# Optimization experiments

Measured on AMD Instinct MI355X. Metric: run time of the kernel, lower is better.

Reference implementation:

```python
import jax, jax.numpy as jnp
import numpy as np
from jax import lax

# ---- model dims ----
NTOKEN = 60697
D_MODEL = 512
NLAYERS = 4
D_STATE = 16
D_CONV = 4
EXPAND = 2
D_INNER = EXPAND * D_MODEL      # 1024
DT_RANK = (D_MODEL + 15) // 16  # 32 (ceil(d_model/16), mamba default)
B_SZ = 4
SEQ = 2048
EPS = 1e-5


def setup_inputs() -> dict:
    key = jax.random.key(0)
    ks = jax.random.split(key, 16)
    s = 0.02
    src = jax.random.randint(ks[0], (B_SZ, SEQ), 0, NTOKEN)
    src_key_padding_mask = jnp.ones((B_SZ, SEQ), dtype=bool)
    emb_w = jax.random.normal(ks[1], (NTOKEN, D_MODEL), jnp.float32) * s
    enc_ln_w = jnp.ones((D_MODEL,), jnp.float32)
    enc_ln_b = jnp.zeros((D_MODEL,), jnp.float32)
    ln_w = jnp.ones((NLAYERS, D_MODEL), jnp.float32)
    ln_b = jnp.zeros((NLAYERS, D_MODEL), jnp.float32)
    in_proj_w = jax.random.normal(ks[2], (NLAYERS, 2 * D_INNER, D_MODEL), jnp.float32) * s
    conv_w = jax.random.normal(ks[3], (NLAYERS, D_INNER, D_CONV), jnp.float32) * 0.1
    conv_b = jnp.zeros((NLAYERS, D_INNER), jnp.float32)
    x_proj_w = jax.random.normal(ks[4], (NLAYERS, DT_RANK + 2 * D_STATE, D_INNER), jnp.float32) * s
    dt_proj_w = jax.random.normal(ks[5], (NLAYERS, D_INNER, DT_RANK), jnp.float32) * (DT_RANK ** -0.5)
    dt_proj_b = jax.random.uniform(ks[6], (NLAYERS, D_INNER), jnp.float32, -4.0, -2.0)
    # S4D real init: A = -[1..d_state], stored as log
    A_log = jnp.log(jnp.broadcast_to(jnp.arange(1, D_STATE + 1, dtype=jnp.float32),
                                     (NLAYERS, D_INNER, D_STATE)))
    D_skip = jnp.ones((NLAYERS, D_INNER), jnp.float32)
    out_proj_w = jax.random.normal(ks[7], (NLAYERS, D_MODEL, D_INNER), jnp.float32) * s / np.sqrt(NLAYERS)
    normf_w = jnp.ones((D_MODEL,), jnp.float32)
    normf_b = jnp.zeros((D_MODEL,), jnp.float32)
    return {
        'src': src, 'src_key_padding_mask': src_key_padding_mask,
        'emb_w': emb_w, 'enc_ln_w': enc_ln_w, 'enc_ln_b': enc_ln_b,
        'ln_w': ln_w, 'ln_b': ln_b, 'in_proj_w': in_proj_w,
        'conv_w': conv_w, 'conv_b': conv_b, 'x_proj_w': x_proj_w,
        'dt_proj_w': dt_proj_w, 'dt_proj_b': dt_proj_b,
        'A_log': A_log, 'D_skip': D_skip, 'out_proj_w': out_proj_w,
        'normf_w': normf_w, 'normf_b': normf_b,
    }


def _layer_norm(x, w, b, eps=EPS):
    mu = jnp.mean(x, axis=-1, keepdims=True)
    var = jnp.mean(jnp.square(x - mu), axis=-1, keepdims=True)
    return (x - mu) * lax.rsqrt(var + eps) * w + b


def _mamba_mixer(h, in_w, cw, cb, xw, dtw, dtb, A_log, D_skip, ow):
    B, L, _ = h.shape
    xz = h @ in_w.T                                   # [B,L,2*d_inner]
    x, z = jnp.split(xz, 2, axis=-1)
    # causal depthwise conv1d, kernel D_CONV
    xt = x.swapaxes(1, 2)                             # [B,d_inner,L]
    xp = jnp.pad(xt, ((0, 0), (0, 0), (D_CONV - 1, 0)))
    conv = cb[None, :, None]
    for k in range(D_CONV):
        conv = conv + cw[:, k][None, :, None] * xp[:, :, k:k + L]
    x = jax.nn.silu(conv).swapaxes(1, 2)              # [B,L,d_inner]
    xdbl = x @ xw.T                                   # [B,L,dt_rank+2*d_state]
    dt = jax.nn.softplus(xdbl[..., :DT_RANK] @ dtw.T + dtb)      # [B,L,d_inner]
    Bm = xdbl[..., DT_RANK:DT_RANK + D_STATE]                    # [B,L,d_state]
    Cm = xdbl[..., DT_RANK + D_STATE:]                           # [B,L,d_state]
    A = -jnp.exp(A_log)                               # [d_inner,d_state]

    def step(hst, inp):
        dt_t, b_t, c_t, x_t = inp                     # [B,d_inner],[B,d_state],[B,d_state],[B,d_inner]
        dA = jnp.exp(dt_t[..., None] * A)             # [B,d_inner,d_state]
        hst = dA * hst + (dt_t * x_t)[..., None] * b_t[:, None, :]
        y_t = jnp.einsum('bds,bs->bd', hst, c_t)
        return hst, y_t

    xs = (dt.swapaxes(0, 1), Bm.swapaxes(0, 1), Cm.swapaxes(0, 1), x.swapaxes(0, 1))
    h0 = jnp.zeros((B, D_INNER, D_STATE), dtype=h.dtype)
    _, ys = lax.scan(step, h0, xs)                    # ys: [L,B,d_inner]
    y = ys.swapaxes(0, 1) + x * D_skip
    y = y * jax.nn.silu(z)
    return y @ ow.T


def reference(src, src_key_padding_mask, emb_w, enc_ln_w, enc_ln_b, ln_w, ln_b,
              in_proj_w, conv_w, conv_b, x_proj_w, dt_proj_w, dt_proj_b,
              A_log, D_skip, out_proj_w, normf_w, normf_b):
    # GeneEncoder: embedding -> LayerNorm (dropout = identity in eval)
    hidden = _layer_norm(emb_w[src], enc_ln_w, enc_ln_b)
    residual = None
    for i in range(NLAYERS):  # prenorm Mamba Blocks
        residual = hidden if residual is None else hidden + residual
        hidden = _mamba_mixer(_layer_norm(residual, ln_w[i], ln_b[i]),
                              in_proj_w[i], conv_w[i], conv_b[i], x_proj_w[i],
                              dt_proj_w[i], dt_proj_b[i], A_log[i], D_skip[i],
                              out_proj_w[i])
    residual = hidden + residual
    return _layer_norm(residual, normf_w, normf_b)
```

## Files before the change

### kernel.cpp

```cpp
#include <hip/hip_runtime.h>
#include <hip/hip_bf16.h>
#include <math.h>

#define NTOKEN 60697
#define D_MODEL 512
#define NLAYERS 4
#define D_STATE 16
#define D_CONV 4
#define D_INNER 1024
#define DT_RANK 32
#define B_SZ 4
#define SEQ 2048
#define EPS 1e-5f
#define NROWS (B_SZ * SEQ)
#define CHUNK 128
#define NCHUNK (SEQ / CHUNK)
#define LOG2E 1.44269504f

typedef __bf16 bf16_t;
typedef __attribute__((ext_vector_type(8))) __bf16 bfx8;
typedef __attribute__((ext_vector_type(4))) __bf16 bfx4;
typedef __attribute__((ext_vector_type(4))) float f32x4;


__device__ __forceinline__ float fast_sigmoid(float x) {
    return 1.0f / (1.0f + __expf(-x));
}
__device__ __forceinline__ float silu(float x) {
    return x * fast_sigmoid(x);
}
__device__ __forceinline__ float softplus_f(float x) {
    return (x > 20.0f) ? x : log1pf(__expf(x));
}
__device__ __forceinline__ float exp2_fast(float x) {
    float r;
    asm("v_exp_f32 %0, %1" : "=v"(r) : "v"(x));
    return r;
}
__device__ __forceinline__ unsigned int bf16bits(float v) {
    return (unsigned int)__builtin_bit_cast(unsigned short, (bf16_t)v);
}
__device__ __forceinline__ float lo16f(unsigned int u) {
    return __builtin_bit_cast(float, u << 16);
}
__device__ __forceinline__ float hi16f(unsigned int u) {
    return __builtin_bit_cast(float, u & 0xFFFF0000u);
}

__device__ __forceinline__ void gload_lds16(const void* g, void* l) {
    __builtin_amdgcn_global_load_lds(
        (const __attribute__((address_space(1))) unsigned int*)g,
        (__attribute__((address_space(3))) unsigned int*)l, 16, 0, 0);
}

template <int CTRL>
__device__ __forceinline__ float dpp_fetch(float x) {
    int xi = __builtin_bit_cast(int, x);
    int yi = __builtin_amdgcn_update_dpp(0, xi, CTRL, 0xF, 0xF, true);
    return __builtin_bit_cast(float, yi);
}
__device__ __forceinline__ float dpp_sum16(float p) {
    p += dpp_fetch<0xB1>(p);
    p += dpp_fetch<0x4E>(p);
    p += dpp_fetch<0x141>(p);
    p += dpp_fetch<0x140>(p);
    return p;
}

__device__ __forceinline__ float blk_reduce_sum(float x, float* sbuf) {
#pragma unroll
    for (int m = 32; m >= 1; m >>= 1) x += __shfl_xor(x, m);
    int wid = threadIdx.x >> 6;
    if ((threadIdx.x & 63) == 0) sbuf[wid] = x;
    __syncthreads();
    float t = sbuf[0] + sbuf[1] + sbuf[2] + sbuf[3];
    __syncthreads();
    return t;
}

__global__ __launch_bounds__(256) void cast_bf16_kernel(
    const float* __restrict__ in, bf16_t* __restrict__ out, size_t n)
{
    size_t stride = (size_t)gridDim.x * 256 * 4;
    for (size_t i = ((size_t)blockIdx.x * 256 + threadIdx.x) * 4; i < n; i += stride) {
        float4 v = *reinterpret_cast<const float4*>(in + i);
        bfx4 o;
        o[0] = (bf16_t)v.x; o[1] = (bf16_t)v.y;
        o[2] = (bf16_t)v.z; o[3] = (bf16_t)v.w;
        *reinterpret_cast<bfx4*>(out + i) = o;
    }
}


__global__ __launch_bounds__(256) void embed_ln_kernel(
    const int* __restrict__ src, const float* __restrict__ emb,
    const float* __restrict__ w, const float* __restrict__ b,
    float* __restrict__ R)
{
    __shared__ float sbuf[4];
    int row = blockIdx.x;
    int tok = src[row];
    const float* e = emb + (size_t)tok * D_MODEL;
    int c0 = threadIdx.x, c1 = threadIdx.x + 256;
    float v0 = e[c0], v1 = e[c1];
    float mu = blk_reduce_sum(v0 + v1, sbuf) * (1.0f / D_MODEL);
    float d0 = v0 - mu, d1 = v1 - mu;
    float var = blk_reduce_sum(d0 * d0 + d1 * d1, sbuf) * (1.0f / D_MODEL);
    float rs = rsqrtf(var + EPS);
    size_t base = (size_t)row * D_MODEL;
    R[base + c0] = d0 * rs * w[c0] + b[c0];
    R[base + c1] = d1 * rs * w[c1] + b[c1];
}

__global__ __launch_bounds__(256) void add_ln_kernel(
    float* __restrict__ R, const float* __restrict__ Hadd,
    const float* __restrict__ w, const float* __restrict__ b,
    float* __restrict__ out, bf16_t* __restrict__ outb)
{
    __shared__ float sbuf[4];
    size_t base = (size_t)blockIdx.x * D_MODEL;
    int c0 = threadIdx.x, c1 = c0 + 256;
    float v0 = R[base + c0], v1 = R[base + c1];
    if (Hadd) {
        v0 += Hadd[base + c0];
        v1 += Hadd[base + c1];
        R[base + c0] = v0;
        R[base + c1] = v1;
    }
    float mu = blk_reduce_sum(v0 + v1, sbuf) * (1.0f / D_MODEL);
    float d0 = v0 - mu, d1 = v1 - mu;
    float var = blk_reduce_sum(d0 * d0 + d1 * d1, sbuf) * (1.0f / D_MODEL);
    float rs = rsqrtf(var + EPS);
    float o0 = d0 * rs * w[c0] + b[c0];
    float o1 = d1 * rs * w[c1] + b[c1];
    if (out) {
        out[base + c0] = o0;
        out[base + c1] = o1;
    }
    if (outb) {
        outb[base + c0] = (bf16_t)o0;
        outb[base + c1] = (bf16_t)o1;
    }
}

template <int EPI>
__global__ __launch_bounds__(256) void gemm_bf16_nt(
    const bf16_t* __restrict__ A, const bf16_t* __restrict__ B,
    float* __restrict__ C, int ldc, int K, const float* __restrict__ bias,
    const unsigned short* __restrict__ xcb_u16,
    unsigned int* __restrict__ dtx_u32,
    bf16_t* __restrict__ Cxb, bf16_t* __restrict__ Czb)
{
    __shared__ bf16_t As[128 * 32];
    __shared__ bf16_t Bs[128 * 32];
    int tid = threadIdx.x;
    int lane = tid & 63, wid = tid >> 6;
    int m0 = blockIdx.y * 128, n0 = blockIdx.x * 128;
    int wm = (wid >> 1) * 64, wn = (wid & 1) * 64;
    int c_lo = lane & 15;
    int khalf = lane >> 4;

    f32x4 acc[4][4];
#pragma unroll
    for (int i = 0; i < 4; i++)
#pragma unroll
        for (int j = 0; j < 4; j++)
            acc[i][j] = (f32x4){0.f, 0.f, 0.f, 0.f};

    for (int k0 = 0; k0 < K; k0 += 32) {
#pragma unroll
        for (int i = 0; i < 2; i++) {
            int c = i * 256 + tid;
            int row = c >> 2;
            int cb = (c & 3) * 16;
            int ldsoff = (i * 256 + wid * 64) * 16;
            gload_lds16((const char*)A + ((size_t)(m0 + row) * K + k0) * 2 + cb,
                        (char*)As + ldsoff);
            gload_lds16((const char*)B + ((size_t)(n0 + row) * K + k0) * 2 + cb,
                        (char*)Bs + ldsoff);
        }
        __syncthreads();

        bfx8 af[4], bfr[4];
#pragma unroll
        for (int i = 0; i < 4; i++) {
            af[i]  = *reinterpret_cast<const bfx8*>(As + (wm + i * 16 + c_lo) * 32 + khalf * 8);
            bfr[i] = *reinterpret_cast<const bfx8*>(Bs + (wn + i * 16 + c_lo) * 32 + khalf * 8);
        }
#pragma unroll
        for (int i = 0; i < 4; i++)
#pragma unroll
            for (int j = 0; j < 4; j++)
                acc[i][j] = __builtin_amdgcn_mfma_f32_16x16x32_bf16(af[i], bfr[j], acc[i][j], 0, 0, 0);
        __syncthreads();
    }

#pragma unroll
    for (int i = 0; i < 4; i++) {
#pragma unroll
        for (int j = 0; j < 4; j++) {
            int row0 = m0 + wm + i * 16 + khalf * 4;
            int col = n0 + wn + j * 16 + c_lo;
#pragma unroll
            for (int r = 0; r < 4; r++) {
                int row = row0 + r;
                float v = acc[i][j][r];
                if (EPI == 0) {
                    C[(size_t)row * ldc + col] = v;
                } else if (EPI == 2) {
                    v = softplus_f(v + bias[col]);
                    float xf = lo16f((unsigned int)xcb_u16[(size_t)row * D_INNER + col]);
                    unsigned int u = bf16bits(v) | (bf16bits(v * xf) << 16);
                    dtx_u32[(size_t)(row >> 1) * 2048 + col * 2 + (row & 1)] = u;
                } else if (EPI == 3) {
                    if (col < D_INNER) Cxb[(size_t)row * D_INNER + col] = (bf16_t)v;
                    else               Czb[(size_t)row * D_INNER + col - D_INNER] = (bf16_t)v;
                }
            }
        }
    }
}

__global__ __launch_bounds__(128) void gemm_xp_bf16(
    const bf16_t* __restrict__ A, const bf16_t* __restrict__ Bmat,
    bf16_t* __restrict__ XDlow, unsigned int* __restrict__ BCb, int K)
{
    __shared__ bf16_t As[64 * 32];
    __shared__ bf16_t Bs[64 * 32];
    int tid = threadIdx.x;
    int lane = tid & 63, w = tid >> 6;
    int m0 = blockIdx.x * 64;
    int wr0 = w * 32;
    int c_lo = lane & 15;
    int khalf = lane >> 4;

    f32x4 acc[2][4];
#pragma unroll
    for (int i = 0; i < 2; i++)
#pragma unroll
        for (int j = 0; j < 4; j++)
            acc[i][j] = (f32x4){0.f, 0.f, 0.f, 0.f};

    for (int k0 = 0; k0 < K; k0 += 32) {
#pragma unroll
        for (int call = 0; call < 2; call++) {
            int c = call * 128 + tid;
            int base = (call * 128 + w * 64) * 16;
            gload_lds16((const char*)A + ((size_t)(m0 + (c >> 2)) * K + k0) * 2 + (c & 3) * 16,
                        (char*)As + base);
            gload_lds16((const char*)Bmat + ((size_t)(c >> 2) * K + k0) * 2 + (c & 3) * 16,
                        (char*)Bs + base);
        }
        __syncthreads();

        bfx8 af[2], bfr[4];
#pragma unroll
        for (int i = 0; i < 2; i++)
            af[i] = *reinterpret_cast<const bfx8*>(As + (wr0 + i * 16 + c_lo) * 32 + khalf * 8);
#pragma unroll
        for (int j = 0; j < 4; j++)
            bfr[j] = *reinterpret_cast<const bfx8*>(Bs + (j * 16 + c_lo) * 32 + khalf * 8);
#pragma unroll
        for (int i = 0; i < 2; i++)
#pragma unroll
            for (int j = 0; j < 4; j++)
                acc[i][j] = __builtin_amdgcn_mfma_f32_16x16x32_bf16(af[i], bfr[j], acc[i][j], 0, 0, 0);
        __syncthreads();
    }

#pragma unroll
    for (int i = 0; i < 2; i++) {
        int row0 = m0 + wr0 + i * 16 + khalf * 4;
#pragma unroll
        for (int r = 0; r < 4; r++) {
            int row = row0 + r;
            XDlow[(size_t)row * DT_RANK + c_lo]      = (bf16_t)acc[i][0][r];
            XDlow[(size_t)row * DT_RANK + 16 + c_lo] = (bf16_t)acc[i][1][r];
            unsigned int u = bf16bits(acc[i][2][r]) | (bf16bits(acc[i][3][r]) << 16);
            BCb[(size_t)(row >> 1) * 32 + c_lo * 2 + (row & 1)] = u;
        }
    }
}

__global__ __launch_bounds__(256) void conv_silu_kernel(
    const bf16_t* __restrict__ Xrawb, const float* __restrict__ cw,
    const float* __restrict__ cb, bf16_t* __restrict__ XCb)
{
    size_t gid = (size_t)blockIdx.x * 256 + threadIdx.x;
    int d = (int)(gid & (D_INNER - 1));
    size_t bt = gid >> 10;
    int t = (int)(bt & (SEQ - 1));
    float acc = cb[d];
#pragma unroll
    for (int k = 0; k < D_CONV; k++) {
        int tt = t + k - (D_CONV - 1);
        if (tt >= 0)
            acc += cw[d * D_CONV + k] * (float)Xrawb[(bt + (size_t)(k - (D_CONV - 1))) * D_INNER + d];
    }
    XCb[gid] = (bf16_t)silu(acc);
}

__device__ __forceinline__ void scan_stage64(
    char* base, const unsigned int* __restrict__ DTXp,
    const unsigned int* __restrict__ BCp, size_t rowpair0, int d0, int tid)
{
    gload_lds16(DTXp + (rowpair0 + (size_t)(tid >> 3)) * 2048 + d0 * 2 + (tid & 7) * 4,
                base + tid * 16);
    gload_lds16(BCp + rowpair0 * 32 + tid * 4, base + 4096 + tid * 16);
}

__global__ __launch_bounds__(256) void scan_pA_kernel(
    const unsigned int* __restrict__ DTXb, const unsigned int* __restrict__ BCb,
    const float* __restrict__ A_log,
    float* __restrict__ DcB, float* __restrict__ UcB)
{
    __shared__ __align__(16) char lds[2][8192];
    const int tid = threadIdx.x;
    const int s = tid & 15, dl = tid >> 4;
    const int b = blockIdx.x >> 6;
    const int d0 = (blockIdx.x & 63) * 16;
    const int c = blockIdx.y;
    const int d = d0 + dl;
    const float Av2 = -__expf(A_log[d * D_STATE + s]) * LOG2E;
    const size_t bbase = (size_t)b * SEQ;
    const int tstart = c * CHUNK;

    float h = 0.f, cum = 0.f;
    scan_stage64(lds[0], DTXb, BCb, (bbase + tstart) >> 1, d0, tid);
    __syncthreads();
    int cur = 0;
    for (int t0 = 0; t0 < CHUNK; t0 += 64) {
        if (t0 + 64 < CHUNK)
            scan_stage64(lds[cur ^ 1], DTXb, BCb, (bbase + tstart + t0 + 64) >> 1, d0, tid);
        const char* L = lds[cur];
#pragma unroll
        for (int kk2 = 0; kk2 < 32; kk2++) {
            uint2 dp = *(const uint2*)(L + kk2 * 128 + dl * 8);
            uint2 bp = *(const uint2*)(L + 4096 + kk2 * 128 + s * 8);
#pragma unroll
            for (int j = 0; j < 2; j++) {
                unsigned int pk = j ? dp.y : dp.x;
                unsigned int bk = j ? bp.y : bp.x;
                float dtv = lo16f(pk);
                float ux  = hi16f(pk);
                float bv  = lo16f(bk);
                float e = exp2_fast(dtv * Av2);
                h = fmaf(e, h, ux * bv);
                cum += dtv;
            }
        }
        __syncthreads();
        cur ^= 1;
    }
    size_t cb64 = ((size_t)c * B_SZ + b) * D_INNER + d;
    UcB[cb64 * 16 + s] = h;
    if (s == 0) DcB[cb64] = cum;
}

__global__ __launch_bounds__(256) void scan_p2_kernel(
    const float* __restrict__ A_log, const float* __restrict__ DcB,
    const float* __restrict__ UcB, float* __restrict__ HcB)
{
    int tid = threadIdx.x;
    int s = tid & 15, dl = tid >> 4;
    int chain = blockIdx.x * 16 + dl;
    int b = chain >> 10, d = chain & 1023;
    float Av = -__expf(A_log[d * D_STATE + s]);
    float Hv = 0.f;
    for (int c = 0; c < NCHUNK; c++) {
        size_t base = ((size_t)c * B_SZ + b) * D_INNER + d;
        HcB[base * 16 + s] = Hv;
        Hv = __expf(Av * DcB[base]) * Hv + UcB[base * 16 + s];
    }
}

__global__ __launch_bounds__(256) void scan_pB_kernel(
    const unsigned int* __restrict__ DTXb, const unsigned int* __restrict__ BCb,
    const float* __restrict__ HcB, const float* __restrict__ A_log,
    const bf16_t* __restrict__ Zbufb, const float* __restrict__ Dskip,
    bf16_t* __restrict__ XCb)
{
    __shared__ __align__(16) char lds[2][8192];
    __shared__ float ytile[32][17];
    const int tid = threadIdx.x;
    const int s = tid & 15, dl = tid >> 4;
    const int b = blockIdx.x >> 6;
    const int d0 = (blockIdx.x & 63) * 16;
    const int c = blockIdx.y;
    const int d = d0 + dl;
    const float Av2 = -__expf(A_log[d * D_STATE + s]) * LOG2E;
    const size_t bbase = (size_t)b * SEQ;
    const int tstart = c * CHUNK;

    float h = HcB[(((size_t)c * B_SZ + b) * D_INNER + d) * 16 + s];

    const int tl  = tid >> 3;
    const int dlo = (tid * 2) & 15;
    const float dsk0 = Dskip[d0 + dlo];
    const float dsk1 = Dskip[d0 + dlo + 1];

    scan_stage64(lds[0], DTXb, BCb, (bbase + tstart) >> 1, d0, tid);
    __syncthreads();
    int cur = 0;
    for (int t0 = 0; t0 < CHUNK; t0 += 64) {
        if (t0 + 64 < CHUNK)
            scan_stage64(lds[cur ^ 1], DTXb, BCb, (bbase + tstart + t0 + 64) >> 1, d0, tid);
        const char* L = lds[cur];
#pragma unroll
        for (int g = 0; g < 2; g++) {
#pragma unroll
            for (int half = 0; half < 2; half++) {
                float yhold = 0.f;
#pragma unroll
                for (int k8 = 0; k8 < 8; k8++) {
                    int kk2 = g * 16 + half * 8 + k8;
                    uint2 dp = *(const uint2*)(L + kk2 * 128 + dl * 8);
                    uint2 bp = *(const uint2*)(L + 4096 + kk2 * 128 + s * 8);
#pragma unroll
                    for (int j = 0; j < 2; j++) {
                        unsigned int pk = j ? dp.y : dp.x;
                        unsigned int bk = j ? bp.y : bp.x;
                        float dtv = lo16f(pk);
                        float ux  = hi16f(pk);
                        float bv  = lo16f(bk);
                        float cv  = hi16f(bk);
                        float e = exp2_fast(dtv * Av2);
                        h = fmaf(e, h, ux * bv);
                        float p = dpp_sum16(h * cv);
                        if (s == k8 * 2 + j + half * 0) {  }
                        int k16 = k8 * 2 + j;
                        if (s == k16) yhold = p;
                    }
                }
                ytile[half * 16 + s][dl] = yhold;
            }
            __syncthreads();
            {
                int t = tstart + t0 + g * 32 + tl;
                size_t row = (bbase + t) * (size_t)D_INNER + d0 + dlo;
                float y0 = ytile[tl][dlo];
                float y1 = ytile[tl][dlo + 1];
                unsigned int xw = *(const unsigned int*)(XCb + row);
                unsigned int zw = *(const unsigned int*)(Zbufb + row);
                float g0 = (y0 + lo16f(xw) * dsk0) * silu(lo16f(zw));
                float g1 = (y1 + hi16f(xw) * dsk1) * silu(hi16f(zw));
                unsigned int o = bf16bits(g0) | (bf16bits(g1) << 16);
                *(unsigned int*)(XCb + row) = o;
            }
            __syncthreads();
        }
        cur ^= 1;
    }
}


extern "C" void kernel_launch(void* const* d_in, const int* in_sizes, int n_in,
                              void* d_out, int out_size, void* d_ws, size_t ws_size,
                              hipStream_t stream) {
    const int*   src       = (const int*)d_in[0];
    const float* emb_w     = (const float*)d_in[2];
    const float* enc_ln_w  = (const float*)d_in[3];
    const float* enc_ln_b  = (const float*)d_in[4];
    const float* ln_w      = (const float*)d_in[5];
    const float* ln_b      = (const float*)d_in[6];
    const float* in_proj_w = (const float*)d_in[7];
    const float* conv_w    = (const float*)d_in[8];
    const float* conv_b    = (const float*)d_in[9];
    const float* x_proj_w  = (const float*)d_in[10];
    const float* dt_proj_w = (const float*)d_in[11];
    const float* dt_proj_b = (const float*)d_in[12];
    const float* A_log     = (const float*)d_in[13];
    const float* D_skip    = (const float*)d_in[14];
    const float* out_proj_w= (const float*)d_in[15];
    const float* normf_w   = (const float*)d_in[16];
    const float* normf_b   = (const float*)d_in[17];
    float* out = (float*)d_out;

    float* R    = (float*)d_ws;
    float* H    = R    + (size_t)NROWS * D_MODEL;
    float* DcB  = H    + (size_t)NROWS * D_MODEL;
    float* UcB  = DcB  + (size_t)NCHUNK * B_SZ * D_INNER;
    float* HcB  = UcB  + (size_t)NCHUNK * B_SZ * D_INNER * D_STATE;
    unsigned int* BCb = (unsigned int*)(HcB + (size_t)NCHUNK * B_SZ * D_INNER * D_STATE);
    unsigned int* DTXb = BCb + (size_t)(NROWS / 2) * 32;
    bf16_t* Hb    = (bf16_t*)(DTXb + (size_t)(NROWS / 2) * 2048);
    bf16_t* Xrawb = Hb    + (size_t)NROWS * D_MODEL;
    bf16_t* Zbufb = Xrawb + (size_t)NROWS * D_INNER;
    bf16_t* XCb   = Zbufb + (size_t)NROWS * D_INNER;
    bf16_t* XDlow = XCb   + (size_t)NROWS * D_INNER;
    bf16_t* Wib   = XDlow + (size_t)NROWS * DT_RANK;
    bf16_t* Wob   = Wib   + (size_t)NLAYERS * 2 * D_INNER * D_MODEL;
    bf16_t* xpb   = Wob   + (size_t)NLAYERS * D_MODEL * D_INNER;
    bf16_t* dtwb  = xpb   + (size_t)NLAYERS * 64 * D_INNER;

    cast_bf16_kernel<<<2048, 256, 0, stream>>>(in_proj_w, Wib, (size_t)NLAYERS * 2 * D_INNER * D_MODEL);
    cast_bf16_kernel<<<2048, 256, 0, stream>>>(out_proj_w, Wob, (size_t)NLAYERS * D_MODEL * D_INNER);
    cast_bf16_kernel<<<256, 256, 0, stream>>>(x_proj_w, xpb, (size_t)NLAYERS * 64 * D_INNER);
    cast_bf16_kernel<<<128, 256, 0, stream>>>(dt_proj_w, dtwb, (size_t)NLAYERS * D_INNER * DT_RANK);

    embed_ln_kernel<<<NROWS, 256, 0, stream>>>(src, emb_w, enc_ln_w, enc_ln_b, R);

    for (int L = 0; L < NLAYERS; L++) {
        const float* AlogL = A_log + (size_t)L * D_INNER * D_STATE;

        add_ln_kernel<<<NROWS, 256, 0, stream>>>(
            R, (L == 0) ? nullptr : H, ln_w + L * D_MODEL, ln_b + L * D_MODEL,
            nullptr, Hb);

        gemm_bf16_nt<3><<<dim3(16, 64), 256, 0, stream>>>(
            Hb, Wib + (size_t)L * 2 * D_INNER * D_MODEL, nullptr, 0, D_MODEL,
            nullptr, nullptr, nullptr, Xrawb, Zbufb);

        conv_silu_kernel<<<(NROWS * D_INNER) / 256, 256, 0, stream>>>(
            Xrawb, conv_w + (size_t)L * D_INNER * D_CONV, conv_b + (size_t)L * D_INNER, XCb);

        gemm_xp_bf16<<<NROWS / 64, 128, 0, stream>>>(
            XCb, xpb + (size_t)L * 64 * D_INNER, XDlow, BCb, D_INNER);

        gemm_bf16_nt<2><<<dim3(8, 64), 256, 0, stream>>>(
            XDlow, dtwb + (size_t)L * D_INNER * DT_RANK, nullptr, 0, DT_RANK,
            dt_proj_b + (size_t)L * D_INNER, (const unsigned short*)XCb, DTXb,
            nullptr, nullptr);

        scan_pA_kernel<<<dim3(B_SZ * 64, NCHUNK), 256, 0, stream>>>(
            DTXb, BCb, AlogL, DcB, UcB);
        scan_p2_kernel<<<256, 256, 0, stream>>>(AlogL, DcB, UcB, HcB);
        scan_pB_kernel<<<dim3(B_SZ * 64, NCHUNK), 256, 0, stream>>>(
            DTXb, BCb, HcB, AlogL, Zbufb, D_skip + (size_t)L * D_INNER, XCb);

        gemm_bf16_nt<0><<<dim3(4, 64), 256, 0, stream>>>(
            XCb, Wob + (size_t)L * D_MODEL * D_INNER, H, D_MODEL, D_INNER,
            nullptr, nullptr, nullptr, nullptr, nullptr);
    }

    add_ln_kernel<<<NROWS, 256, 0, stream>>>(R, H, normf_w, normf_b, out, nullptr);
}
```

Baseline: 1.084 ms.

## Fold inter-chunk scan prefix into scan_pB, vectorize conv, use inline DPP adds

Removes the separate scan_p2 kernel: each scan_pB block now recomputes its chunk's starting state by serially combining the prior chunks' (Dc, Uc) summaries, overlapped with the first LDS stage load. This drops one launch and the HcB write/read round trip, but adds redundant sequential work that grows with the chunk index. The conv+SiLU kernel now handles two bf16 channels per thread with 32-bit loads and stores. The 16-lane DPP reduction is rewritten as inline v_add_f32_dpp asm so each shuffle fuses with its add.

```diff
diff --git a/kernel.cpp b/kernel.cpp
--- a/kernel.cpp
+++ b/kernel.cpp
@@ -53,17 +53,16 @@
         (__attribute__((address_space(3))) unsigned int*)l, 16, 0, 0);
 }
 
-template <int CTRL>
-__device__ __forceinline__ float dpp_fetch(float x) {
-    int xi = __builtin_bit_cast(int, x);
-    int yi = __builtin_amdgcn_update_dpp(0, xi, CTRL, 0xF, 0xF, true);
-    return __builtin_bit_cast(float, yi);
-}
 __device__ __forceinline__ float dpp_sum16(float p) {
-    p += dpp_fetch<0xB1>(p);
-    p += dpp_fetch<0x4E>(p);
-    p += dpp_fetch<0x141>(p);
-    p += dpp_fetch<0x140>(p);
+    float t;
+    asm("v_add_f32_dpp %0, %1, %1 quad_perm:[1,0,3,2] row_mask:0xf bank_mask:0xf"
+        : "=v"(t) : "v"(p));
+    asm("v_add_f32_dpp %0, %1, %1 quad_perm:[2,3,0,1] row_mask:0xf bank_mask:0xf"
+        : "=v"(p) : "v"(t));
+    asm("v_add_f32_dpp %0, %1, %1 row_half_mirror row_mask:0xf bank_mask:0xf"
+        : "=v"(t) : "v"(p));
+    asm("v_add_f32_dpp %0, %1, %1 row_mirror row_mask:0xf bank_mask:0xf"
+        : "=v"(p) : "v"(t));
     return p;
 }
 
@@ -287,17 +286,23 @@
     const float* __restrict__ cb, bf16_t* __restrict__ XCb)
 {
     size_t gid = (size_t)blockIdx.x * 256 + threadIdx.x;
-    int d = (int)(gid & (D_INNER - 1));
-    size_t bt = gid >> 10;
+    int dp = (int)(gid & 511);
+    size_t bt = gid >> 9;
     int t = (int)(bt & (SEQ - 1));
-    float acc = cb[d];
+    const unsigned int* Xu = (const unsigned int*)Xrawb;
+    int d0 = 2 * dp;
+    float a0 = cb[d0], a1 = cb[d0 + 1];
 #pragma unroll
     for (int k = 0; k < D_CONV; k++) {
         int tt = t + k - (D_CONV - 1);
-        if (tt >= 0)
-            acc += cw[d * D_CONV + k] * (float)Xrawb[(bt + (size_t)(k - (D_CONV - 1))) * D_INNER + d];
-    }
-    XCb[gid] = (bf16_t)silu(acc);
+        if (tt >= 0) {
+            unsigned int u = Xu[(bt + (size_t)(k - (D_CONV - 1))) * 512 + dp];
+            a0 += cw[d0 * D_CONV + k] * lo16f(u);
+            a1 += cw[(d0 + 1) * D_CONV + k] * hi16f(u);
+        }
+    }
+    unsigned int o = bf16bits(silu(a0)) | (bf16bits(silu(a1)) << 16);
+    ((unsigned int*)XCb)[gid] = o;
 }
 
 __device__ __forceinline__ void scan_stage64(
@@ -357,26 +362,10 @@
     if (s == 0) DcB[cb64] = cum;
 }
 
-__global__ __launch_bounds__(256) void scan_p2_kernel(
-    const float* __restrict__ A_log, const float* __restrict__ DcB,
-    const float* __restrict__ UcB, float* __restrict__ HcB)
-{
-    int tid = threadIdx.x;
-    int s = tid & 15, dl = tid >> 4;
-    int chain = blockIdx.x * 16 + dl;
-    int b = chain >> 10, d = chain & 1023;
-    float Av = -__expf(A_log[d * D_STATE + s]);
-    float Hv = 0.f;
-    for (int c = 0; c < NCHUNK; c++) {
-        size_t base = ((size_t)c * B_SZ + b) * D_INNER + d;
-        HcB[base * 16 + s] = Hv;
-        Hv = __expf(Av * DcB[base]) * Hv + UcB[base * 16 + s];
-    }
-}
-
 __global__ __launch_bounds__(256) void scan_pB_kernel(
     const unsigned int* __restrict__ DTXb, const unsigned int* __restrict__ BCb,
-    const float* __restrict__ HcB, const float* __restrict__ A_log,
+    const float* __restrict__ DcB, const float* __restrict__ UcB,
+    const float* __restrict__ A_log,
     const bf16_t* __restrict__ Zbufb, const float* __restrict__ Dskip,
     bf16_t* __restrict__ XCb)
 {
@@ -392,14 +381,19 @@
     const size_t bbase = (size_t)b * SEQ;
     const int tstart = c * CHUNK;
 
-    float h = HcB[(((size_t)c * B_SZ + b) * D_INNER + d) * 16 + s];
+    scan_stage64(lds[0], DTXb, BCb, (bbase + tstart) >> 1, d0, tid);
+
+    float h = 0.f;
+    for (int j = 0; j < c; j++) {
+        size_t base = ((size_t)j * B_SZ + b) * D_INNER + d;
+        h = exp2_fast(Av2 * DcB[base]) * h + UcB[base * 16 + s];
+    }
 
     const int tl  = tid >> 3;
     const int dlo = (tid * 2) & 15;
     const float dsk0 = Dskip[d0 + dlo];
     const float dsk1 = Dskip[d0 + dlo + 1];
 
-    scan_stage64(lds[0], DTXb, BCb, (bbase + tstart) >> 1, d0, tid);
     __syncthreads();
     int cur = 0;
     for (int t0 = 0; t0 < CHUNK; t0 += 64) {
@@ -427,7 +421,6 @@
                         float e = exp2_fast(dtv * Av2);
                         h = fmaf(e, h, ux * bv);
                         float p = dpp_sum16(h * cv);
-                        if (s == k8 * 2 + j + half * 0) {  }
                         int k16 = k8 * 2 + j;
                         if (s == k16) yhold = p;
                     }
@@ -480,8 +473,7 @@
     float* H    = R    + (size_t)NROWS * D_MODEL;
     float* DcB  = H    + (size_t)NROWS * D_MODEL;
     float* UcB  = DcB  + (size_t)NCHUNK * B_SZ * D_INNER;
-    float* HcB  = UcB  + (size_t)NCHUNK * B_SZ * D_INNER * D_STATE;
-    unsigned int* BCb = (unsigned int*)(HcB + (size_t)NCHUNK * B_SZ * D_INNER * D_STATE);
+    unsigned int* BCb = (unsigned int*)(UcB + (size_t)NCHUNK * B_SZ * D_INNER * D_STATE);
     unsigned int* DTXb = BCb + (size_t)(NROWS / 2) * 32;
     bf16_t* Hb    = (bf16_t*)(DTXb + (size_t)(NROWS / 2) * 2048);
     bf16_t* Xrawb = Hb    + (size_t)NROWS * D_MODEL;
@@ -511,7 +503,7 @@
             Hb, Wib + (size_t)L * 2 * D_INNER * D_MODEL, nullptr, 0, D_MODEL,
             nullptr, nullptr, nullptr, Xrawb, Zbufb);
 
-        conv_silu_kernel<<<(NROWS * D_INNER) / 256, 256, 0, stream>>>(
+        conv_silu_kernel<<<(NROWS * D_INNER / 2) / 256, 256, 0, stream>>>(
             Xrawb, conv_w + (size_t)L * D_INNER * D_CONV, conv_b + (size_t)L * D_INNER, XCb);
 
         gemm_xp_bf16<<<NROWS / 64, 128, 0, stream>>>(
@@ -524,9 +516,8 @@
 
         scan_pA_kernel<<<dim3(B_SZ * 64, NCHUNK), 256, 0, stream>>>(
             DTXb, BCb, AlogL, DcB, UcB);
-        scan_p2_kernel<<<256, 256, 0, stream>>>(AlogL, DcB, UcB, HcB);
         scan_pB_kernel<<<dim3(B_SZ * 64, NCHUNK), 256, 0, stream>>>(
-            DTXb, BCb, HcB, AlogL, Zbufb, D_skip + (size_t)L * D_INNER, XCb);
+            DTXb, BCb, DcB, UcB, AlogL, Zbufb, D_skip + (size_t)L * D_INNER, XCb);
 
         gemm_bf16_nt<0><<<dim3(4, 64), 256, 0, stream>>>(
             XCb, Wob + (size_t)L * D_MODEL * D_INNER, H, D_MODEL, D_INNER,
```

Measured after the change: 1.151 ms. +6.2%, slower.
